# Performance work log

Hardware: AMD Instinct MI355X
Metric: run time of the kernel (lower is better)

## Reference

```python
import jax, jax.numpy as jnp
import numpy as np

B, R, S, C, H, MLP = 4, 32, 4, 128, 4, 512  # batch, resolution, box_size, dim, heads, mlp_dim
N = S ** 3            # tokens per window = 64
NW = (R // S) ** 3    # windows per batch element = 512
SHIFT = S // 2


def _layernorm(x, g, b):
    m = jnp.mean(x, axis=-1, keepdims=True)
    v = jnp.var(x, axis=-1, keepdims=True)
    return (x - m) * jax.lax.rsqrt(v + 1e-5) * g + b


def _box_partition(x):
    # x: (b, R, R, R, C) -> (b*NW, N, C)
    b = x.shape[0]
    x = x.reshape(b, R // S, S, R // S, S, R // S, S, C)
    x = x.transpose(0, 1, 3, 5, 2, 4, 6, 7)
    return x.reshape(-1, N, C)


def _box_reverse(w, b):
    # w: (b*NW, N, C) -> (b, R, R, R, C)
    x = w.reshape(b, R // S, R // S, R // S, S, S, S, C)
    x = x.transpose(0, 1, 4, 2, 5, 3, 6, 7)
    return x.reshape(b, R, R, R, C)


def setup_inputs():
    key = jax.random.key(0)
    ks = jax.random.split(key, 8)
    f = lambda k, sh: jax.random.normal(k, sh, dtype=jnp.float32) * 0.02
    x = jax.random.normal(ks[0], (B, R ** 3, C), dtype=jnp.float32)
    qkv_w = f(ks[1], (3 * C, C))
    rpb_table = f(ks[2], ((3 * S - 1) ** 3, H))
    proj_w = f(ks[3], (C, C))
    proj_b = jnp.zeros((C,), jnp.float32)
    norm1_g = jnp.ones((C,), jnp.float32)
    norm1_b = jnp.zeros((C,), jnp.float32)
    norm2_g = jnp.ones((C,), jnp.float32)
    norm2_b = jnp.zeros((C,), jnp.float32)
    mlp_w1 = f(ks[4], (MLP, C))
    mlp_b1 = jnp.zeros((MLP,), jnp.float32)
    mlp_w2 = f(ks[5], (C, MLP))
    mlp_b2 = jnp.zeros((C,), jnp.float32)
    # relative position index (N, N), int constant
    coords = np.stack(np.meshgrid(*([np.arange(S)] * 3), indexing='ij')).reshape(3, -1)
    rel = coords[:, :, None] - coords[:, None, :]
    rel = rel.transpose(1, 2, 0) + (S - 1)
    rel[..., 0] *= (2 * S - 1) ** 2
    rel[..., 1] *= (2 * S - 1)
    rel_index = jnp.asarray(rel.sum(-1), jnp.int32)
    # shifted-window additive attention mask (NW, N, N)
    img = np.zeros((1, R, R, R, 1), np.float32)
    sl = (slice(0, -S), slice(-S, -SHIFT), slice(-SHIFT, None))
    cnt = 0
    for a in sl:
        for b2 in sl:
            for c in sl:
                img[:, a, b2, c, :] = cnt
                cnt += 1
    m = img.reshape(1, R // S, S, R // S, S, R // S, S, 1)
    m = m.transpose(0, 1, 3, 5, 2, 4, 6, 7).reshape(-1, N)
    am = m[:, None, :] - m[:, :, None]
    attn_mask = jnp.asarray(np.where(am != 0, -100.0, 0.0).astype(np.float32))
    return dict(x=x, qkv_w=qkv_w, rpb_table=rpb_table, proj_w=proj_w, proj_b=proj_b,
                norm1_g=norm1_g, norm1_b=norm1_b, norm2_g=norm2_g, norm2_b=norm2_b,
                mlp_w1=mlp_w1, mlp_b1=mlp_b1, mlp_w2=mlp_w2, mlp_b2=mlp_b2,
                attn_mask=attn_mask, rel_index=rel_index)


def reference(x, qkv_w, rpb_table, proj_w, proj_b, norm1_g, norm1_b,
              norm2_g, norm2_b, mlp_w1, mlp_b1, mlp_w2, mlp_b2,
              attn_mask, rel_index):
    scale = (C // H) ** -0.5
    shortcut = x
    xn = _layernorm(x, norm1_g, norm1_b).reshape(B, R, R, R, C)
    xs = jnp.roll(xn, (-SHIFT,) * 3, axis=(1, 2, 3))
    w = _box_partition(xs)  # (B*NW, N, C)
    qkv = (w @ qkv_w.T).reshape(-1, N, 3, H, C // H).transpose(2, 0, 3, 1, 4)
    q, k, v = qkv[0] * scale, qkv[1], qkv[2]  # (B*NW, H, N, hd)
    attn = jnp.einsum('whnd,whmd->whnm', q, k)
    bias = rpb_table[rel_index].transpose(2, 0, 1)  # (H, N, N)
    attn = attn + bias[None]
    attn = attn.reshape(B, NW, H, N, N) + attn_mask[None, :, None]
    attn = jax.nn.softmax(attn.reshape(-1, H, N, N), axis=-1)
    out = jnp.einsum('whnm,whmd->whnd', attn, v).transpose(0, 2, 1, 3).reshape(-1, N, C)
    out = out @ proj_w.T + proj_b
    xm = _box_reverse(out, B)
    xm = jnp.roll(xm, (SHIFT,) * 3, axis=(1, 2, 3)).reshape(B, -1, C)
    x1 = shortcut + 0.5 * xm
    h = _layernorm(x1, norm2_g, norm2_b)
    h = jax.nn.gelu(h @ mlp_w1.T + mlp_b1, approximate=False) @ mlp_w2.T + mlp_b2
    return x1 + 0.5 * h
```

## Files before the change

kernel.cpp:

```cpp
#include <hip/hip_runtime.h>

typedef unsigned short u16;
typedef unsigned int u32;
typedef short bf16x8 __attribute__((ext_vector_type(8)));
typedef float f32x4 __attribute__((ext_vector_type(4)));

__device__ __forceinline__ u16 f2bf(float f) {
  union { float f; u32 i; } v; v.f = f;
  u32 x = v.i;
  x += 0x7fff + ((x >> 16) & 1);
  return (u16)(x >> 16);
}
__device__ __forceinline__ u32 pack2(float a, float b) {
  return (u32)f2bf(a) | ((u32)f2bf(b) << 16);
}


__global__ void prep_kernel(const float* __restrict__ rpb, const int* __restrict__ rel,
                            const float* __restrict__ qkv_w, const float* __restrict__ proj_w,
                            const float* __restrict__ w1, const float* __restrict__ w2,
                            float* __restrict__ bias, u16* __restrict__ qkv_f,
                            u16* __restrict__ proj_f, u16* __restrict__ w1f,
                            u16* __restrict__ w2f) {
  const int bid = blockIdx.x;
  if (bid < 64) {
    const int idx = bid * 256 + threadIdx.x;
    const int h = idx >> 12, rm = idx & 4095;
    bias[idx] = rpb[rel[rm] * 4 + h];
    return;
  }
  const int i4 = (bid - 64) * 256 + threadIdx.x;
  const int e = i4 * 4;
  const float scale = 0.17677669529663687f;
  float4 v; u16* dst;
  if (e < 49152) {
    v = *(const float4*)(qkv_w + e);
    if (e < 16384) { v.x *= scale; v.y *= scale; v.z *= scale; v.w *= scale; }
    const int row = e >> 7, col = e & 127;
    const int tile = (row >> 4) * 4 + (col >> 5);
    const int lane = ((col >> 3) & 3) * 16 + (row & 15);
    dst = qkv_f + tile * 512 + lane * 8 + (col & 7);
  } else if (e < 65536) {
    const int le = e - 49152;
    v = *(const float4*)(proj_w + le);
    const int row = le >> 7, col = le & 127;
    const int tile = (row >> 4) * 4 + (col >> 5);
    const int lane = ((col >> 3) & 3) * 16 + (row & 15);
    dst = proj_f + tile * 512 + lane * 8 + (col & 7);
  } else if (e < 131072) {
    const int le = e - 65536;
    v = *(const float4*)(w1 + le);
    const int row = le >> 7, col = le & 127;
    const int tile = (row >> 4) * 4 + (col >> 5);
    const int lane = ((col >> 3) & 3) * 16 + (row & 15);
    dst = w1f + tile * 512 + lane * 8 + (col & 7);
  } else {
    const int le = e - 131072;
    v = *(const float4*)(w2 + le);
    const int row = le >> 9, col = le & 511;
    const int tile = (row >> 4) * 16 + (col >> 5);
    const int lane = ((col >> 3) & 3) * 16 + (row & 15);
    dst = w2f + tile * 512 + lane * 8 + (col & 7);
  }
  *(uint2*)dst = make_uint2(pack2(v.x, v.y), pack2(v.z, v.w));
}

__global__ __launch_bounds__(512, 4) void attn_kernel(
    const float* __restrict__ x, const u16* __restrict__ qkv_f,
    const u16* __restrict__ proj_f, const float* __restrict__ proj_b,
    const float* __restrict__ n1g, const float* __restrict__ n1b,
    const float* __restrict__ amask, const float* __restrict__ bias,
    float* __restrict__ out)
{
  __shared__ __align__(16) unsigned char lds[70656];
  __shared__ int srcIdx[64];
  u16* xw = (u16*)(lds);
  u16* qb = (u16*)(lds + 17408);
  u16* kb = (u16*)(lds + 34816);
  u16* vt = (u16*)(lds + 52224);
  unsigned char* Pb = lds;
  u16* Ob = kb;

  const int tid = threadIdx.x;
  const int wv = tid >> 6, lane = tid & 63;
  const int l15 = lane & 15, lg = lane >> 4;
  const int hw = wv & 3;
  const int half = wv >> 2;

  const int wIdx = blockIdx.x;
  const int bb = wIdx >> 9, ww = wIdx & 511;
  const int w0 = ww >> 6, w1i = (ww >> 3) & 7, w2i = ww & 7;

  {
    const int tok = tid >> 3;
    const int qt = tid & 7;
    const int s0 = tok >> 4, s1 = (tok >> 2) & 3, s2 = tok & 3;
    const int p0 = (w0 * 4 + s0 + 2) & 31;
    const int p1 = (w1i * 4 + s1 + 2) & 31;
    const int p2 = (w2i * 4 + s2 + 2) & 31;
    const int src = (bb << 15) + (p0 << 10) + (p1 << 5) + p2;
    if (qt == 0) srcIdx[tok] = src;
    float v[16]; float s = 0.f, sq = 0.f;
    const float4* p4 = (const float4*)(x + src * 128 + qt * 16);
    #pragma unroll
    for (int i = 0; i < 4; ++i) {
      float4 u = p4[i];
      v[i * 4 + 0] = u.x; v[i * 4 + 1] = u.y; v[i * 4 + 2] = u.z; v[i * 4 + 3] = u.w;
      s += u.x + u.y + u.z + u.w;
      sq += u.x * u.x + u.y * u.y + u.z * u.z + u.w * u.w;
    }
    s  += __shfl_xor(s, 1);  s  += __shfl_xor(s, 2);  s  += __shfl_xor(s, 4);
    sq += __shfl_xor(sq, 1); sq += __shfl_xor(sq, 2); sq += __shfl_xor(sq, 4);
    const float mean = s * 0.0078125f;
    const float var  = sq * 0.0078125f - mean * mean;
    const float rstd = rsqrtf(var + 1e-5f);
    u16* dst = xw + tok * 136 + qt * 16;
    #pragma unroll
    for (int i = 0; i < 16; i += 2) {
      const int c = qt * 16 + i;
      float y0 = (v[i]     - mean) * rstd * n1g[c]     + n1b[c];
      float y1 = (v[i + 1] - mean) * rstd * n1g[c + 1] + n1b[c + 1];
      *(u32*)(dst + i) = pack2(y0, y1);
    }
  }
  __syncthreads();

  const f32x4 zero4 = {0.f, 0.f, 0.f, 0.f};

  bf16x8 xa[2][4];
  #pragma unroll
  for (int ti = 0; ti < 2; ++ti)
    #pragma unroll
    for (int ks = 0; ks < 4; ++ks)
      xa[ti][ks] = *(const bf16x8*)(xw + ((half * 2 + ti) * 16 + l15) * 136 + ks * 32 + lg * 8);

  #pragma unroll
  for (int cc = 0; cc < 2; ++cc) {
    const u16* wp = qkv_f + (cc * 4 + hw) * 4 * 512 + lane * 8;
    f32x4 acc[2] = {zero4, zero4};
    #pragma unroll
    for (int ks = 0; ks < 4; ++ks) {
      const bf16x8 bfr = *(const bf16x8*)(wp + ks * 512);
      acc[0] = __builtin_amdgcn_mfma_f32_16x16x32_bf16(xa[0][ks], bfr, acc[0], 0, 0, 0);
      acc[1] = __builtin_amdgcn_mfma_f32_16x16x32_bf16(xa[1][ks], bfr, acc[1], 0, 0, 0);
    }
    const int o = cc * 64 + hw * 16 + l15;
    #pragma unroll
    for (int ti = 0; ti < 2; ++ti)
      #pragma unroll
      for (int r = 0; r < 4; ++r)
        qb[((half * 2 + ti) * 16 + lg * 4 + r) * 136 + o] = f2bf(acc[ti][r]);
  }
  #pragma unroll
  for (int cc = 2; cc < 4; ++cc) {
    const u16* wp = qkv_f + (cc * 4 + hw) * 4 * 512 + lane * 8;
    f32x4 acc[2] = {zero4, zero4};
    #pragma unroll
    for (int ks = 0; ks < 4; ++ks) {
      const bf16x8 bfr = *(const bf16x8*)(wp + ks * 512);
      acc[0] = __builtin_amdgcn_mfma_f32_16x16x32_bf16(xa[0][ks], bfr, acc[0], 0, 0, 0);
      acc[1] = __builtin_amdgcn_mfma_f32_16x16x32_bf16(xa[1][ks], bfr, acc[1], 0, 0, 0);
    }
    const int o = (cc - 2) * 64 + hw * 16 + l15;
    #pragma unroll
    for (int ti = 0; ti < 2; ++ti)
      #pragma unroll
      for (int r = 0; r < 4; ++r)
        kb[((half * 2 + ti) * 16 + lg * 4 + r) * 136 + o] = f2bf(acc[ti][r]);
  }
  #pragma unroll
  for (int cc = 4; cc < 6; ++cc) {
    const u16* wp = qkv_f + (cc * 4 + hw) * 4 * 512 + lane * 8;
    f32x4 acc[2] = {zero4, zero4};
    #pragma unroll
    for (int ks = 0; ks < 4; ++ks) {
      const bf16x8 bfr = *(const bf16x8*)(wp + ks * 512);
      acc[0] = __builtin_amdgcn_mfma_f32_16x16x32_bf16(xa[0][ks], bfr, acc[0], 0, 0, 0);
      acc[1] = __builtin_amdgcn_mfma_f32_16x16x32_bf16(xa[1][ks], bfr, acc[1], 0, 0, 0);
    }
    const int cvch = (cc - 4) * 64 + hw * 16 + l15;
    #pragma unroll
    for (int ti = 0; ti < 2; ++ti) {
      uint2 pk = make_uint2(pack2(acc[ti][0], acc[ti][1]), pack2(acc[ti][2], acc[ti][3]));
      *(uint2*)(vt + cvch * 72 + (half * 2 + ti) * 16 + lg * 4) = pk;
    }
  }
  __syncthreads();

  f32x4 s[2][4];
  {
    bf16x8 qa[2];
    #pragma unroll
    for (int ti = 0; ti < 2; ++ti)
      qa[ti] = *(const bf16x8*)(qb + ((half * 2 + ti) * 16 + l15) * 136 + hw * 32 + lg * 8);
    #pragma unroll
    for (int tj = 0; tj < 4; ++tj) {
      const bf16x8 kf = *(const bf16x8*)(kb + (tj * 16 + l15) * 136 + hw * 32 + lg * 8);
      s[0][tj] = __builtin_amdgcn_mfma_f32_16x16x32_bf16(qa[0], kf, zero4, 0, 0, 0);
      s[1][tj] = __builtin_amdgcn_mfma_f32_16x16x32_bf16(qa[1], kf, zero4, 0, 0, 0);
    }
  }
  #pragma unroll
  for (int ti = 0; ti < 2; ++ti) {
    #pragma unroll
    for (int r = 0; r < 4; ++r) {
      const int row = (half * 2 + ti) * 16 + lg * 4 + r;
      const float* bp = bias + hw * 4096 + row * 64;
      const float* mp = amask + ww * 4096 + row * 64;
      #pragma unroll
      for (int tj = 0; tj < 4; ++tj) {
        const int col = tj * 16 + l15;
        s[ti][tj][r] += bp[col] + mp[col];
      }
    }
  }
  __syncthreads();

  unsigned char* ps = Pb + wv * 4096;
  float rcp[2][4];
  #pragma unroll
  for (int ti = 0; ti < 2; ++ti) {
    #pragma unroll
    for (int r = 0; r < 4; ++r) {
      float mx = fmaxf(fmaxf(s[ti][0][r], s[ti][1][r]), fmaxf(s[ti][2][r], s[ti][3][r]));
      mx = fmaxf(mx, __shfl_xor(mx, 1));
      mx = fmaxf(mx, __shfl_xor(mx, 2));
      mx = fmaxf(mx, __shfl_xor(mx, 4));
      mx = fmaxf(mx, __shfl_xor(mx, 8));
      float sum = 0.f;
      #pragma unroll
      for (int tj = 0; tj < 4; ++tj) {
        float e = __expf(s[ti][tj][r] - mx);
        s[ti][tj][r] = e; sum += e;
      }
      sum += __shfl_xor(sum, 1);
      sum += __shfl_xor(sum, 2);
      sum += __shfl_xor(sum, 4);
      sum += __shfl_xor(sum, 8);
      rcp[ti][r] = 1.0f / sum;
      const int row = ti * 16 + lg * 4 + r;
      const int swz = (row & 7) << 4;
      #pragma unroll
      for (int tj = 0; tj < 4; ++tj) {
        const int byteoff = (row * 128 + (tj * 16 + l15) * 2) ^ swz;
        *(u16*)(ps + byteoff) = f2bf(s[ti][tj][r]);
      }
    }
  }

  {
    f32x4 oacc[2][2] = {{zero4, zero4}, {zero4, zero4}};
    #pragma unroll
    for (int ks = 0; ks < 2; ++ks) {
      bf16x8 pa[2], vb[2];
      #pragma unroll
      for (int ti = 0; ti < 2; ++ti) {
        const int row = ti * 16 + l15;
        const int slot = ((ks * 4 + lg) ^ (row & 7)) << 4;
        pa[ti] = *(const bf16x8*)(ps + row * 128 + slot);
      }
      #pragma unroll
      for (int tj = 0; tj < 2; ++tj)
        vb[tj] = *(const bf16x8*)(vt + (hw * 32 + tj * 16 + l15) * 72 + ks * 32 + lg * 8);
      #pragma unroll
      for (int ti = 0; ti < 2; ++ti)
        #pragma unroll
        for (int tj = 0; tj < 2; ++tj)
          oacc[ti][tj] = __builtin_amdgcn_mfma_f32_16x16x32_bf16(pa[ti], vb[tj], oacc[ti][tj], 0, 0, 0);
    }
    #pragma unroll
    for (int ti = 0; ti < 2; ++ti)
      #pragma unroll
      for (int tj = 0; tj < 2; ++tj)
        #pragma unroll
        for (int r = 0; r < 4; ++r) {
          const int tok = (half * 2 + ti) * 16 + lg * 4 + r;
          Ob[tok * 136 + hw * 32 + tj * 16 + l15] = f2bf(oacc[ti][tj][r] * rcp[ti][r]);
        }
  }
  __syncthreads();

  bf16x8 oafr[2][4];
  #pragma unroll
  for (int ti = 0; ti < 2; ++ti)
    #pragma unroll
    for (int ks = 0; ks < 4; ++ks)
      oafr[ti][ks] = *(const bf16x8*)(Ob + ((half * 2 + ti) * 16 + l15) * 136 + ks * 32 + lg * 8);
  #pragma unroll
  for (int cc = 0; cc < 2; ++cc) {
    const u16* wp = proj_f + (cc * 4 + hw) * 4 * 512 + lane * 8;
    f32x4 acc[2] = {zero4, zero4};
    #pragma unroll
    for (int ks = 0; ks < 4; ++ks) {
      const bf16x8 bfr = *(const bf16x8*)(wp + ks * 512);
      acc[0] = __builtin_amdgcn_mfma_f32_16x16x32_bf16(oafr[0][ks], bfr, acc[0], 0, 0, 0);
      acc[1] = __builtin_amdgcn_mfma_f32_16x16x32_bf16(oafr[1][ks], bfr, acc[1], 0, 0, 0);
    }
    const int c = cc * 64 + hw * 16 + l15;
    const float pbv = proj_b[c];
    #pragma unroll
    for (int ti = 0; ti < 2; ++ti) {
      #pragma unroll
      for (int r = 0; r < 4; ++r) {
        const int tok = (half * 2 + ti) * 16 + lg * 4 + r;
        const int src = srcIdx[tok];
        out[src * 128 + c] = x[src * 128 + c] + 0.5f * (acc[ti][r] + pbv);
      }
    }
  }
}

__global__ __launch_bounds__(256, 4) void mlp_kernel(
    const u16* __restrict__ w1f, const float* __restrict__ b1,
    const u16* __restrict__ w2f, const float* __restrict__ b2,
    const float* __restrict__ n2g, const float* __restrict__ n2b,
    float* __restrict__ out)
{
  __shared__ __align__(16) unsigned char lds[35840];
  u16* xn  = (u16*)(lds);
  u16* h1c0 = (u16*)(lds + 17408);
  u16* h1c1 = (u16*)(lds + 26624);

  const int tid = threadIdx.x;
  const int wave = tid >> 6, lane = tid & 63;
  const int l15 = lane & 15, lg = lane >> 4;
  const int base = blockIdx.x * 64;
  const f32x4 zero4 = {0.f, 0.f, 0.f, 0.f};

  {
    const int tl = tid >> 2;
    const int qt = tid & 3;
    const int tokg = base + tl;
    float v[32]; float s = 0.f, sq = 0.f;
    const float4* p4 = (const float4*)(out + tokg * 128 + qt * 32);
    #pragma unroll
    for (int i = 0; i < 8; ++i) {
      float4 u = p4[i];
      v[i * 4 + 0] = u.x; v[i * 4 + 1] = u.y; v[i * 4 + 2] = u.z; v[i * 4 + 3] = u.w;
      s += u.x + u.y + u.z + u.w;
      sq += u.x * u.x + u.y * u.y + u.z * u.z + u.w * u.w;
    }
    s  += __shfl_xor(s, 1);  s  += __shfl_xor(s, 2);
    sq += __shfl_xor(sq, 1); sq += __shfl_xor(sq, 2);
    const float mean = s * 0.0078125f;
    const float var  = sq * 0.0078125f - mean * mean;
    const float rstd = rsqrtf(var + 1e-5f);
    u16* dst = xn + tl * 136 + qt * 32;
    #pragma unroll
    for (int i = 0; i < 32; i += 2) {
      const int c = qt * 32 + i;
      float y0 = (v[i]     - mean) * rstd * n2g[c]     + n2b[c];
      float y1 = (v[i + 1] - mean) * rstd * n2g[c + 1] + n2b[c + 1];
      *(u32*)(dst + i) = pack2(y0, y1);
    }
  }
  __syncthreads();

  f32x4 acc2[4][2];
  #pragma unroll
  for (int ti = 0; ti < 4; ++ti) { acc2[ti][0] = zero4; acc2[ti][1] = zero4; }

  #pragma unroll 1
  for (int oc = 0; oc < 8; ++oc) {
    u16* h1c = (oc & 1) ? h1c1 : h1c0;
    f32x4 a1[4];
    #pragma unroll
    for (int t = 0; t < 4; ++t) a1[t] = zero4;
    const u16* wp1 = w1f + (oc * 4 + wave) * 4 * 512 + lane * 8;
    #pragma unroll
    for (int ks = 0; ks < 4; ++ks) {
      const bf16x8 bfr = *(const bf16x8*)(wp1 + ks * 512);
      #pragma unroll
      for (int ti = 0; ti < 4; ++ti) {
        const bf16x8 afr = *(const bf16x8*)(xn + (ti * 16 + l15) * 136 + ks * 32 + lg * 8);
        a1[ti] = __builtin_amdgcn_mfma_f32_16x16x32_bf16(afr, bfr, a1[ti], 0, 0, 0);
      }
    }
    bf16x8 w2r[2][2];
    #pragma unroll
    for (int tj = 0; tj < 2; ++tj)
      #pragma unroll
      for (int ks = 0; ks < 2; ++ks)
        w2r[tj][ks] = *(const bf16x8*)(w2f + (((wave * 2 + tj) * 16) + (oc * 2 + ks)) * 512 + lane * 8);

    const int ol = wave * 16 + l15;
    const float b1v = b1[oc * 64 + ol];
    #pragma unroll
    for (int ti = 0; ti < 4; ++ti) {
      #pragma unroll
      for (int r = 0; r < 4; ++r) {
        const int tok = ti * 16 + lg * 4 + r;
        const float u = a1[ti][r] + b1v;
        const float t = u + 0.044715f * u * u * u;
        const float ge = u / (1.0f + __expf(-1.5957691216057308f * t));
        h1c[tok * 72 + ol] = f2bf(ge);
      }
    }
    __syncthreads();

    #pragma unroll
    for (int ks = 0; ks < 2; ++ks) {
      bf16x8 afr[4];
      #pragma unroll
      for (int ti = 0; ti < 4; ++ti)
        afr[ti] = *(const bf16x8*)(h1c + (ti * 16 + l15) * 72 + ks * 32 + lg * 8);
      #pragma unroll
      for (int ti = 0; ti < 4; ++ti)
        #pragma unroll
        for (int tj = 0; tj < 2; ++tj)
          acc2[ti][tj] = __builtin_amdgcn_mfma_f32_16x16x32_bf16(afr[ti], w2r[tj][ks], acc2[ti][tj], 0, 0, 0);
    }
  }

  #pragma unroll
  for (int tj = 0; tj < 2; ++tj) {
    const int c = wave * 32 + tj * 16 + l15;
    const float b2v = b2[c];
    #pragma unroll
    for (int ti = 0; ti < 4; ++ti) {
      #pragma unroll
      for (int r = 0; r < 4; ++r) {
        const int tokg = base + ti * 16 + lg * 4 + r;
        out[tokg * 128 + c] += 0.5f * (acc2[ti][tj][r] + b2v);
      }
    }
  }
}

extern "C" void kernel_launch(void* const* d_in, const int* in_sizes, int n_in,
                              void* d_out, int out_size, void* d_ws, size_t ws_size,
                              hipStream_t stream) {
  const float* x      = (const float*)d_in[0];
  const float* qkv_w  = (const float*)d_in[1];
  const float* rpb    = (const float*)d_in[2];
  const float* proj_w = (const float*)d_in[3];
  const float* proj_b = (const float*)d_in[4];
  const float* n1g    = (const float*)d_in[5];
  const float* n1b    = (const float*)d_in[6];
  const float* n2g    = (const float*)d_in[7];
  const float* n2b    = (const float*)d_in[8];
  const float* w1     = (const float*)d_in[9];
  const float* b1     = (const float*)d_in[10];
  const float* w2     = (const float*)d_in[11];
  const float* b2     = (const float*)d_in[12];
  const float* amask  = (const float*)d_in[13];
  const int*   rel    = (const int*)d_in[14];
  float* out  = (float*)d_out;

  unsigned char* ws = (unsigned char*)d_ws;
  float* bias = (float*)(ws);
  u16* qkv_f  = (u16*)(ws + 65536);
  u16* proj_f = (u16*)(ws + 163840);
  u16* w1f    = (u16*)(ws + 196608);
  u16* w2f    = (u16*)(ws + 327680);

  prep_kernel<<<256, 256, 0, stream>>>(rpb, rel, qkv_w, proj_w, w1, w2,
                                       bias, qkv_f, proj_f, w1f, w2f);
  attn_kernel<<<2048, 512, 0, stream>>>(x, qkv_f, proj_f, proj_b, n1g, n1b, amask, bias, out);
  mlp_kernel<<<2048, 256, 0, stream>>>(w1f, b1, w2f, b2, n2g, n2b, out);
}
```

Baseline: 161.4 us.

## Transpose MFMA operands for vectorized packed stores, hoist LN tile, fold softmax norm

Swaps the A/B operands of several MFMA calls so each lane's accumulator holds four consecutive channels of one token. This allows packed bf16 (uint2) and float4 global stores in place of scattered scalar writes. Q/K projection loops are merged, the bf16 conversion uses the hardware packed-convert intrinsic, the softmax reciprocal is folded into P before the PV matmul, and the MLP's normalized input is hoisted into registers. The register cache raises pressure, so launch bounds for the MLP kernel drop from 4 to 3 blocks per SM, which may reduce occupancy.

Result: slower. 164.6 us (+2.0%).

```diff
diff --git a/kernel.cpp b/kernel.cpp
--- a/kernel.cpp
+++ b/kernel.cpp
@@ -1,4 +1,5 @@
 #include <hip/hip_runtime.h>
+#include <hip/hip_bf16.h>
 
 typedef unsigned short u16;
 typedef unsigned int u32;
@@ -13,6 +14,10 @@
 }
 __device__ __forceinline__ u32 pack2(float a, float b) {
   return (u32)f2bf(a) | ((u32)f2bf(b) << 16);
+}
+__device__ __forceinline__ u32 cvtpk2(float a, float b) {
+  __hip_bfloat162 t = __float22bfloat162_rn(float2{a, b});
+  union { __hip_bfloat162 h; u32 u; } v; v.h = t; return v.u;
 }
 
 
@@ -120,7 +125,7 @@
       const int c = qt * 16 + i;
       float y0 = (v[i]     - mean) * rstd * n1g[c]     + n1b[c];
       float y1 = (v[i + 1] - mean) * rstd * n1g[c + 1] + n1b[c + 1];
-      *(u32*)(dst + i) = pack2(y0, y1);
+      *(u32*)(dst + i) = cvtpk2(y0, y1);
     }
   }
   __syncthreads();
@@ -135,7 +140,26 @@
       xa[ti][ks] = *(const bf16x8*)(xw + ((half * 2 + ti) * 16 + l15) * 136 + ks * 32 + lg * 8);
 
   #pragma unroll
-  for (int cc = 0; cc < 2; ++cc) {
+  for (int cc = 0; cc < 4; ++cc) {
+    const u16* wp = qkv_f + (cc * 4 + hw) * 4 * 512 + lane * 8;
+    f32x4 acc[2] = {zero4, zero4};
+    #pragma unroll
+    for (int ks = 0; ks < 4; ++ks) {
+      const bf16x8 bfr = *(const bf16x8*)(wp + ks * 512);
+      acc[0] = __builtin_amdgcn_mfma_f32_16x16x32_bf16(bfr, xa[0][ks], acc[0], 0, 0, 0);
+      acc[1] = __builtin_amdgcn_mfma_f32_16x16x32_bf16(bfr, xa[1][ks], acc[1], 0, 0, 0);
+    }
+    u16* dstbuf = (cc < 2) ? qb : kb;
+    const int ob = (cc & 1) * 64 + hw * 16 + lg * 4;
+    #pragma unroll
+    for (int ti = 0; ti < 2; ++ti) {
+      const int token = (half * 2 + ti) * 16 + l15;
+      uint2 pk = make_uint2(cvtpk2(acc[ti][0], acc[ti][1]), cvtpk2(acc[ti][2], acc[ti][3]));
+      *(uint2*)(dstbuf + token * 136 + ob) = pk;
+    }
+  }
+  #pragma unroll
+  for (int cc = 4; cc < 6; ++cc) {
     const u16* wp = qkv_f + (cc * 4 + hw) * 4 * 512 + lane * 8;
     f32x4 acc[2] = {zero4, zero4};
     #pragma unroll
@@ -144,44 +168,10 @@
       acc[0] = __builtin_amdgcn_mfma_f32_16x16x32_bf16(xa[0][ks], bfr, acc[0], 0, 0, 0);
       acc[1] = __builtin_amdgcn_mfma_f32_16x16x32_bf16(xa[1][ks], bfr, acc[1], 0, 0, 0);
     }
-    const int o = cc * 64 + hw * 16 + l15;
-    #pragma unroll
-    for (int ti = 0; ti < 2; ++ti)
-      #pragma unroll
-      for (int r = 0; r < 4; ++r)
-        qb[((half * 2 + ti) * 16 + lg * 4 + r) * 136 + o] = f2bf(acc[ti][r]);
-  }
-  #pragma unroll
-  for (int cc = 2; cc < 4; ++cc) {
-    const u16* wp = qkv_f + (cc * 4 + hw) * 4 * 512 + lane * 8;
-    f32x4 acc[2] = {zero4, zero4};
-    #pragma unroll
-    for (int ks = 0; ks < 4; ++ks) {
-      const bf16x8 bfr = *(const bf16x8*)(wp + ks * 512);
-      acc[0] = __builtin_amdgcn_mfma_f32_16x16x32_bf16(xa[0][ks], bfr, acc[0], 0, 0, 0);
-      acc[1] = __builtin_amdgcn_mfma_f32_16x16x32_bf16(xa[1][ks], bfr, acc[1], 0, 0, 0);
-    }
-    const int o = (cc - 2) * 64 + hw * 16 + l15;
-    #pragma unroll
-    for (int ti = 0; ti < 2; ++ti)
-      #pragma unroll
-      for (int r = 0; r < 4; ++r)
-        kb[((half * 2 + ti) * 16 + lg * 4 + r) * 136 + o] = f2bf(acc[ti][r]);
-  }
-  #pragma unroll
-  for (int cc = 4; cc < 6; ++cc) {
-    const u16* wp = qkv_f + (cc * 4 + hw) * 4 * 512 + lane * 8;
-    f32x4 acc[2] = {zero4, zero4};
-    #pragma unroll
-    for (int ks = 0; ks < 4; ++ks) {
-      const bf16x8 bfr = *(const bf16x8*)(wp + ks * 512);
-      acc[0] = __builtin_amdgcn_mfma_f32_16x16x32_bf16(xa[0][ks], bfr, acc[0], 0, 0, 0);
-      acc[1] = __builtin_amdgcn_mfma_f32_16x16x32_bf16(xa[1][ks], bfr, acc[1], 0, 0, 0);
-    }
     const int cvch = (cc - 4) * 64 + hw * 16 + l15;
     #pragma unroll
     for (int ti = 0; ti < 2; ++ti) {
-      uint2 pk = make_uint2(pack2(acc[ti][0], acc[ti][1]), pack2(acc[ti][2], acc[ti][3]));
+      uint2 pk = make_uint2(cvtpk2(acc[ti][0], acc[ti][1]), cvtpk2(acc[ti][2], acc[ti][3]));
       *(uint2*)(vt + cvch * 72 + (half * 2 + ti) * 16 + lg * 4) = pk;
     }
   }
@@ -217,7 +207,6 @@
   __syncthreads();
 
   unsigned char* ps = Pb + wv * 4096;
-  float rcp[2][4];
   #pragma unroll
   for (int ti = 0; ti < 2; ++ti) {
     #pragma unroll
@@ -237,13 +226,13 @@
       sum += __shfl_xor(sum, 2);
       sum += __shfl_xor(sum, 4);
       sum += __shfl_xor(sum, 8);
-      rcp[ti][r] = 1.0f / sum;
+      const float rcp = 1.0f / sum;
       const int row = ti * 16 + lg * 4 + r;
       const int swz = (row & 7) << 4;
       #pragma unroll
       for (int tj = 0; tj < 4; ++tj) {
         const int byteoff = (row * 128 + (tj * 16 + l15) * 2) ^ swz;
-        *(u16*)(ps + byteoff) = f2bf(s[ti][tj][r]);
+        *(u16*)(ps + byteoff) = f2bf(s[ti][tj][r] * rcp);
       }
     }
   }
@@ -266,17 +255,17 @@
       for (int ti = 0; ti < 2; ++ti)
         #pragma unroll
         for (int tj = 0; tj < 2; ++tj)
-          oacc[ti][tj] = __builtin_amdgcn_mfma_f32_16x16x32_bf16(pa[ti], vb[tj], oacc[ti][tj], 0, 0, 0);
+          oacc[ti][tj] = __builtin_amdgcn_mfma_f32_16x16x32_bf16(vb[tj], pa[ti], oacc[ti][tj], 0, 0, 0);
     }
     #pragma unroll
     for (int ti = 0; ti < 2; ++ti)
       #pragma unroll
-      for (int tj = 0; tj < 2; ++tj)
-        #pragma unroll
-        for (int r = 0; r < 4; ++r) {
-          const int tok = (half * 2 + ti) * 16 + lg * 4 + r;
-          Ob[tok * 136 + hw * 32 + tj * 16 + l15] = f2bf(oacc[ti][tj][r] * rcp[ti][r]);
-        }
+      for (int tj = 0; tj < 2; ++tj) {
+        const int token = (half * 2 + ti) * 16 + l15;
+        uint2 pk = make_uint2(cvtpk2(oacc[ti][tj][0], oacc[ti][tj][1]),
+                              cvtpk2(oacc[ti][tj][2], oacc[ti][tj][3]));
+        *(uint2*)(Ob + token * 136 + hw * 32 + tj * 16 + lg * 4) = pk;
+      }
   }
   __syncthreads();
 
@@ -293,24 +282,26 @@
     #pragma unroll
     for (int ks = 0; ks < 4; ++ks) {
       const bf16x8 bfr = *(const bf16x8*)(wp + ks * 512);
-      acc[0] = __builtin_amdgcn_mfma_f32_16x16x32_bf16(oafr[0][ks], bfr, acc[0], 0, 0, 0);
-      acc[1] = __builtin_amdgcn_mfma_f32_16x16x32_bf16(oafr[1][ks], bfr, acc[1], 0, 0, 0);
-    }
-    const int c = cc * 64 + hw * 16 + l15;
-    const float pbv = proj_b[c];
+      acc[0] = __builtin_amdgcn_mfma_f32_16x16x32_bf16(bfr, oafr[0][ks], acc[0], 0, 0, 0);
+      acc[1] = __builtin_amdgcn_mfma_f32_16x16x32_bf16(bfr, oafr[1][ks], acc[1], 0, 0, 0);
+    }
+    const int cb = cc * 64 + hw * 16 + lg * 4;
+    const float4 pb4 = *(const float4*)(proj_b + cb);
     #pragma unroll
     for (int ti = 0; ti < 2; ++ti) {
-      #pragma unroll
-      for (int r = 0; r < 4; ++r) {
-        const int tok = (half * 2 + ti) * 16 + lg * 4 + r;
-        const int src = srcIdx[tok];
-        out[src * 128 + c] = x[src * 128 + c] + 0.5f * (acc[ti][r] + pbv);
-      }
-    }
-  }
-}
-
-__global__ __launch_bounds__(256, 4) void mlp_kernel(
+      const int token = (half * 2 + ti) * 16 + l15;
+      const int src = srcIdx[token];
+      float4 xr = *(const float4*)(x + src * 128 + cb);
+      xr.x += 0.5f * (acc[ti][0] + pb4.x);
+      xr.y += 0.5f * (acc[ti][1] + pb4.y);
+      xr.z += 0.5f * (acc[ti][2] + pb4.z);
+      xr.w += 0.5f * (acc[ti][3] + pb4.w);
+      *(float4*)(out + src * 128 + cb) = xr;
+    }
+  }
+}
+
+__global__ __launch_bounds__(256, 3) void mlp_kernel(
     const u16* __restrict__ w1f, const float* __restrict__ b1,
     const u16* __restrict__ w2f, const float* __restrict__ b2,
     const float* __restrict__ n2g, const float* __restrict__ n2b,
@@ -351,10 +342,17 @@
       const int c = qt * 32 + i;
       float y0 = (v[i]     - mean) * rstd * n2g[c]     + n2b[c];
       float y1 = (v[i + 1] - mean) * rstd * n2g[c + 1] + n2b[c + 1];
-      *(u32*)(dst + i) = pack2(y0, y1);
+      *(u32*)(dst + i) = cvtpk2(y0, y1);
     }
   }
   __syncthreads();
+
+  bf16x8 xa[4][4];
+  #pragma unroll
+  for (int ti = 0; ti < 4; ++ti)
+    #pragma unroll
+    for (int ks = 0; ks < 4; ++ks)
+      xa[ti][ks] = *(const bf16x8*)(xn + (ti * 16 + l15) * 136 + ks * 32 + lg * 8);
 
   f32x4 acc2[4][2];
   #pragma unroll
@@ -371,10 +369,8 @@
     for (int ks = 0; ks < 4; ++ks) {
       const bf16x8 bfr = *(const bf16x8*)(wp1 + ks * 512);
       #pragma unroll
-      for (int ti = 0; ti < 4; ++ti) {
-        const bf16x8 afr = *(const bf16x8*)(xn + (ti * 16 + l15) * 136 + ks * 32 + lg * 8);
-        a1[ti] = __builtin_amdgcn_mfma_f32_16x16x32_bf16(afr, bfr, a1[ti], 0, 0, 0);
-      }
+      for (int ti = 0; ti < 4; ++ti)
+        a1[ti] = __builtin_amdgcn_mfma_f32_16x16x32_bf16(bfr, xa[ti][ks], a1[ti], 0, 0, 0);
     }
     bf16x8 w2r[2][2];
     #pragma unroll
@@ -383,18 +379,20 @@
       for (int ks = 0; ks < 2; ++ks)
         w2r[tj][ks] = *(const bf16x8*)(w2f + (((wave * 2 + tj) * 16) + (oc * 2 + ks)) * 512 + lane * 8);
 
-    const int ol = wave * 16 + l15;
-    const float b1v = b1[oc * 64 + ol];
+    const int olb = wave * 16 + lg * 4;
+    const float4 b14 = *(const float4*)(b1 + oc * 64 + olb);
+    const float b1v[4] = {b14.x, b14.y, b14.z, b14.w};
     #pragma unroll
     for (int ti = 0; ti < 4; ++ti) {
+      float g[4];
       #pragma unroll
       for (int r = 0; r < 4; ++r) {
-        const int tok = ti * 16 + lg * 4 + r;
-        const float u = a1[ti][r] + b1v;
+        const float u = a1[ti][r] + b1v[r];
         const float t = u + 0.044715f * u * u * u;
-        const float ge = u / (1.0f + __expf(-1.5957691216057308f * t));
-        h1c[tok * 72 + ol] = f2bf(ge);
-      }
+        g[r] = u / (1.0f + __expf(-1.5957691216057308f * t));
+      }
+      const int token = ti * 16 + l15;
+      *(uint2*)(h1c + token * 72 + olb) = make_uint2(cvtpk2(g[0], g[1]), cvtpk2(g[2], g[3]));
     }
     __syncthreads();
 
@@ -408,21 +406,23 @@
       for (int ti = 0; ti < 4; ++ti)
         #pragma unroll
         for (int tj = 0; tj < 2; ++tj)
-          acc2[ti][tj] = __builtin_amdgcn_mfma_f32_16x16x32_bf16(afr[ti], w2r[tj][ks], acc2[ti][tj], 0, 0, 0);
+          acc2[ti][tj] = __builtin_amdgcn_mfma_f32_16x16x32_bf16(w2r[tj][ks], afr[ti], acc2[ti][tj], 0, 0, 0);
     }
   }
 
   #pragma unroll
   for (int tj = 0; tj < 2; ++tj) {
-    const int c = wave * 32 + tj * 16 + l15;
-    const float b2v = b2[c];
+    const int cb = wave * 32 + tj * 16 + lg * 4;
+    const float4 b24 = *(const float4*)(b2 + cb);
     #pragma unroll
     for (int ti = 0; ti < 4; ++ti) {
-      #pragma unroll
-      for (int r = 0; r < 4; ++r) {
-        const int tokg = base + ti * 16 + lg * 4 + r;
-        out[tokg * 128 + c] += 0.5f * (acc2[ti][tj][r] + b2v);
-      }
+      const int tokg = base + ti * 16 + l15;
+      float4 o4 = *(float4*)(out + tokg * 128 + cb);
+      o4.x += 0.5f * (acc2[ti][tj][0] + b24.x);
+      o4.y += 0.5f * (acc2[ti][tj][1] + b24.y);
+      o4.z += 0.5f * (acc2[ti][tj][2] + b24.z);
+      o4.w += 0.5f * (acc2[ti][tj][3] + b24.w);
+      *(float4*)(out + tokg * 128 + cb) = o4;
     }
   }
 }
```
